# Performance work log

Measured on AMD Instinct MI355X. Metric: run time of the kernel, lower is better.

## Reference

```python
import jax, jax.numpy as jnp
import numpy as np

N_NODES = 100000
N_EDGES = 1600000
IN_DIM = 128
OUT_DIM = 64
SLOPE = 0.2


def setup_inputs() -> dict:
    key = jax.random.key(0)
    k1, k2, k3, k4 = jax.random.split(key, 4)
    h = jax.random.normal(k1, (N_NODES, IN_DIM), dtype=jnp.float32)
    W = jax.random.normal(k2, (OUT_DIM, IN_DIM), dtype=jnp.float32) * (1.0 / np.sqrt(IN_DIM))
    src = jax.random.randint(k3, (N_EDGES,), 0, N_NODES, dtype=jnp.int64)
    dst = jax.random.randint(k4, (N_EDGES,), 0, N_NODES, dtype=jnp.int64)
    return {"h": h, "W": W, "src": src, "dst": dst}


def reference(h, W, src, dst):
    n = h.shape[0]
    z = h @ W.T                                   # [N, out_dim]
    z_src = z[src]                                # [E, out_dim]
    z_dst = z[dst]                                # [E, out_dim]
    e = jax.nn.leaky_relu(jnp.sum(z_src * z_dst, axis=1), negative_slope=SLOPE)  # [E]
    # segment softmax over incoming edges of each destination node
    m = jax.ops.segment_max(e, dst, num_segments=n)        # [N], -inf for isolated nodes
    ex = jnp.exp(e - m[dst])                                # [E]
    denom = jax.ops.segment_sum(ex, dst, num_segments=n)    # [N]
    alpha = ex / denom[dst]                                 # [E]
    agg = jax.ops.segment_sum(alpha[:, None] * z_src, dst, num_segments=n)  # [N, out_dim]
    return jax.nn.elu(agg)
```

## Files before the change

kernel.cpp:

```cpp
#include <hip/hip_runtime.h>
#include <hip/hip_fp16.h>
#include <math.h>

#define SLOPE 0.2f
#define LOG2E 1.4426950408889634f

__device__ __forceinline__ unsigned short pk_f16(float x) {
    __half h = __float2half(x);
    return __half_as_ushort(h);
}
__device__ __forceinline__ float f16f(unsigned int bits_lo16) {
    return __half2float(__ushort_as_half((unsigned short)(bits_lo16 & 0xFFFFu)));
}

__global__ __launch_bounds__(256, 8) void gemm_hist_kernel(const float* __restrict__ h,
                                                           const float* __restrict__ W,
                                                           unsigned short* __restrict__ zh,
                                                           const int* __restrict__ dst,
                                                           int* __restrict__ cnt8,
                                                           unsigned short* __restrict__ rank,
                                                           int n, int ne) {
    int g = blockIdx.x / 3;
    int r = blockIdx.x % 3;
    if (r == 2) {
        int* __restrict__ cnt = cnt8 + (size_t)(g & 7) * n;
        int i = g * 256 + threadIdx.x;
        int base = i * 4;
        if (base + 3 < ne) {
            int4 d = *(const int4*)(dst + base);
            unsigned int r0 = atomicAdd(&cnt[d.x], 1);
            unsigned int r1 = atomicAdd(&cnt[d.y], 1);
            unsigned int r2 = atomicAdd(&cnt[d.z], 1);
            unsigned int r3 = atomicAdd(&cnt[d.w], 1);
            uint2 packed;
            packed.x = (r1 << 16) | (r0 & 0xFFFF);
            packed.y = (r3 << 16) | (r2 & 0xFFFF);
            *(uint2*)(rank + base) = packed;
        } else if (base < ne) {
            for (int rr = base; rr < ne; rr++)
                rank[rr] = (unsigned short)atomicAdd(&cnt[dst[rr]], 1);
        }
        return;
    }

    __shared__ float ws[128][36];
    int t = threadIdx.x;
    int gemmIdx = 2 * g + r;
    int nblk = gemmIdx >> 1;
    int ch0  = (gemmIdx & 1) << 5;
    const float4* __restrict__ W4 = reinterpret_cast<const float4*>(W);
#pragma unroll
    for (int j = 0; j < 4; j++) {
        int idx = t + j * 256;
        int o  = idx >> 5;
        int kq = idx & 31;
        float4 w = W4[(size_t)(ch0 + o) * 32 + kq];
        int k = kq << 2;
        int col = o ^ ((kq & 7) << 2);
        ws[k + 0][col] = w.x; ws[k + 1][col] = w.y;
        ws[k + 2][col] = w.z; ws[k + 3][col] = w.w;
    }
    __syncthreads();

    int ng = t >> 3, og = t & 7;
    int n0 = nblk * 64 + ng * 2;
    if (n0 >= n) return;
    const float* __restrict__ hp = h + (size_t)n0 * 128;

    float acc[2][4] = {};
#pragma unroll 4
    for (int k = 0; k < 128; k += 4) {
        int m = (k >> 2) & 7;
        int colb = (og ^ m) << 2;
        float4 hv[2], wv[4];
#pragma unroll
        for (int i = 0; i < 2; i++) hv[i] = *(const float4*)(hp + i * 128 + k);
#pragma unroll
        for (int kk = 0; kk < 4; kk++) wv[kk] = *(const float4*)&ws[k + kk][colb];
#pragma unroll
        for (int i = 0; i < 2; i++) {
            acc[i][0] += hv[i].x * wv[0].x + hv[i].y * wv[1].x + hv[i].z * wv[2].x + hv[i].w * wv[3].x;
            acc[i][1] += hv[i].x * wv[0].y + hv[i].y * wv[1].y + hv[i].z * wv[2].y + hv[i].w * wv[3].y;
            acc[i][2] += hv[i].x * wv[0].z + hv[i].y * wv[1].z + hv[i].z * wv[2].z + hv[i].w * wv[3].z;
            acc[i][3] += hv[i].x * wv[0].w + hv[i].y * wv[1].w + hv[i].z * wv[2].w + hv[i].w * wv[3].w;
        }
    }
#pragma unroll
    for (int i = 0; i < 2; i++) {
        ushort4 o4;
        o4.x = pk_f16(acc[i][0]);
        o4.y = pk_f16(acc[i][1]);
        o4.z = pk_f16(acc[i][2]);
        o4.w = pk_f16(acc[i][3]);
        *(ushort4*)&zh[(size_t)(n0 + i) * 64 + ch0 + og * 4] = o4;
    }
}

__global__ __launch_bounds__(256) void scan1(const int* __restrict__ cnt8,
                                             int* __restrict__ starts,
                                             int* __restrict__ bsums, int n) {
    __shared__ int ls[256];
    int tbase = blockIdx.x * 4096 + threadIdx.x * 16;
    int tot[16];
#pragma unroll
    for (int k = 0; k < 16; k++) tot[k] = 0;
    if (tbase + 15 < n) {
#pragma unroll
        for (int c = 0; c < 8; c++) {
            const int* cp = cnt8 + (size_t)c * n + tbase;
#pragma unroll
            for (int q = 0; q < 4; q++) {
                int4 v = *(const int4*)(cp + q * 4);
                tot[q * 4 + 0] += v.x; tot[q * 4 + 1] += v.y;
                tot[q * 4 + 2] += v.z; tot[q * 4 + 3] += v.w;
            }
        }
    } else {
        for (int k = 0; k < 16; k++) {
            int idx = tbase + k;
            if (idx < n)
                for (int c = 0; c < 8; c++) tot[k] += cnt8[(size_t)c * n + idx];
        }
    }
    int s = 0;
#pragma unroll
    for (int k = 0; k < 16; k++) s += tot[k];
    ls[threadIdx.x] = s;
    __syncthreads();
    for (int off = 1; off < 256; off <<= 1) {
        int t = threadIdx.x >= off ? ls[threadIdx.x - off] : 0;
        __syncthreads();
        ls[threadIdx.x] += t;
        __syncthreads();
    }
    int run = ls[threadIdx.x] - s;
    if (threadIdx.x == 255) bsums[blockIdx.x] = ls[255];
#pragma unroll
    for (int k = 0; k < 16; k++) {
        int idx = tbase + k;
        if (idx < n) starts[idx] = run;
        run += tot[k];
    }
}

__global__ __launch_bounds__(256) void scan3(int* __restrict__ starts,
                                             const int* __restrict__ bsums,
                                             int* __restrict__ cnt8,
                                             int n, int ne) {
    __shared__ int base_s;
    int i = blockIdx.x * 256 + threadIdx.x;
    if (threadIdx.x == 0) {
        int reg = (int)(blockIdx.x >> 4);
        int s = 0;
        for (int b = 0; b < reg; b++) s += bsums[b];
        base_s = s;
        if (blockIdx.x == 0) starts[n] = ne;
    }
    __syncthreads();
    if (i >= n) return;
    int b = starts[i] + base_s;
    starts[i] = b;
#pragma unroll
    for (int c = 0; c < 8; c++) {
        size_t off = (size_t)c * n + i;
        int t = cnt8[off];
        cnt8[off] = b;
        b += t;
    }
}

__global__ __launch_bounds__(256) void scatter8_kernel(const int* __restrict__ src,
                                                       const int* __restrict__ dst,
                                                       const int* __restrict__ cnt8,
                                                       const unsigned short* __restrict__ rank,
                                                       int* __restrict__ csr_src,
                                                       int n, int ne) {
    int i = blockIdx.x * 256 + threadIdx.x;
    int base = i * 8;
    if (base + 7 < ne) {
        const int* __restrict__ cb = cnt8 + (size_t)((base >> 10) & 7) * n;
        int4 s0 = *(const int4*)(src + base),  s1 = *(const int4*)(src + base + 4);
        int4 d0 = *(const int4*)(dst + base),  d1 = *(const int4*)(dst + base + 4);
        uint4 rp = *(const uint4*)(rank + base);
        csr_src[cb[d0.x] + (rp.x & 0xFFFF)] = s0.x;
        csr_src[cb[d0.y] + (rp.x >> 16)]    = s0.y;
        csr_src[cb[d0.z] + (rp.y & 0xFFFF)] = s0.z;
        csr_src[cb[d0.w] + (rp.y >> 16)]    = s0.w;
        csr_src[cb[d1.x] + (rp.z & 0xFFFF)] = s1.x;
        csr_src[cb[d1.y] + (rp.z >> 16)]    = s1.y;
        csr_src[cb[d1.z] + (rp.w & 0xFFFF)] = s1.z;
        csr_src[cb[d1.w] + (rp.w >> 16)]    = s1.w;
    } else {
        for (int e = base; e < ne; e++) {
            const int* cb = cnt8 + (size_t)((e >> 10) & 7) * n;
            csr_src[cb[dst[e]] + rank[e]] = src[e];
        }
    }
}

__global__ __launch_bounds__(256) void fused_node(const uint4* __restrict__ zh4,
                                                  const int* __restrict__ starts,
                                                  const int* __restrict__ csr_src,
                                                  float4* __restrict__ out4, int n) {
    int node = blockIdx.x * 4 + (threadIdx.x >> 6);
    if (node >= n) return;
    int lane = threadIdx.x & 63;
    int g = lane >> 3;
    int q = lane & 7;
    int rs = starts[node], re = starts[node + 1];

    uint4 zw = zh4[(size_t)node * 8 + q];
    float zdf[8];
    zdf[0] = f16f(zw.x); zdf[1] = f16f(zw.x >> 16);
    zdf[2] = f16f(zw.y); zdf[3] = f16f(zw.y >> 16);
    zdf[4] = f16f(zw.z); zdf[5] = f16f(zw.z >> 16);
    zdf[6] = f16f(zw.w); zdf[7] = f16f(zw.w >> 16);

    float m2 = -1e30f, denom = 0.f;
    float acc[8] = {};

    for (int c = rs; c < re; c += 64) {
        int j = c + lane;
        int sv = j < re ? csr_src[j] : 0;
        int cn = min(64, re - c);
        bool val0 = g < cn;
        int  s0 = __shfl(sv, val0 ? g : 0);
        uint4 w0 = zh4[(size_t)s0 * 8 + q];
        bool val1 = 8 + g < cn;
        int  s1 = __shfl(sv, val1 ? 8 + g : 0);
        uint4 w1 = zh4[(size_t)s1 * 8 + q];
        for (int k = 0; k < cn; k += 8) {
            int idx2 = k + 16 + g;
            bool val2 = idx2 < cn;
            int  s2 = __shfl(sv, val2 ? idx2 : 0);
            uint4 w2 = zh4[(size_t)s2 * 8 + q];

            float vf[8];
            vf[0] = f16f(w0.x); vf[1] = f16f(w0.x >> 16);
            vf[2] = f16f(w0.y); vf[3] = f16f(w0.y >> 16);
            vf[4] = f16f(w0.z); vf[5] = f16f(w0.z >> 16);
            vf[6] = f16f(w0.w); vf[7] = f16f(w0.w >> 16);

            float p = vf[0] * zdf[0];
#pragma unroll
            for (int jj = 1; jj < 8; jj++) p = fmaf(vf[jj], zdf[jj], p);
#pragma unroll
            for (int msk = 1; msk < 8; msk <<= 1) p += __shfl_xor(p, msk);

            float e = p > 0.f ? p : SLOPE * p;
            float e2 = e * LOG2E;
            e2 = val0 ? e2 : -2e30f;
            if (__any(e2 > m2)) {
                float mnew = fmaxf(m2, e2);
                float sc = exp2f(m2 - mnew);
                float ex = exp2f(e2 - mnew);
                denom = fmaf(denom, sc, ex);
#pragma unroll
                for (int jj = 0; jj < 8; jj++)
                    acc[jj] = fmaf(acc[jj], sc, ex * vf[jj]);
                m2 = mnew;
            } else {
                float ex = exp2f(e2 - m2);
                denom += ex;
#pragma unroll
                for (int jj = 0; jj < 8; jj++)
                    acc[jj] = fmaf(ex, vf[jj], acc[jj]);
            }
            w0 = w1; val0 = val1;
            w1 = w2; val1 = val2;
        }
    }
#pragma unroll
    for (int msk = 8; msk < 64; msk <<= 1) {
        float mo  = __shfl_xor(m2, msk);
        float dno = __shfl_xor(denom, msk);
        float ao[8];
#pragma unroll
        for (int jj = 0; jj < 8; jj++) ao[jj] = __shfl_xor(acc[jj], msk);
        float mnew = fmaxf(m2, mo);
        float ss = exp2f(m2 - mnew), so = exp2f(mo - mnew);
        denom = fmaf(denom, ss, dno * so);
#pragma unroll
        for (int jj = 0; jj < 8; jj++)
            acc[jj] = fmaf(acc[jj], ss, ao[jj] * so);
        m2 = mnew;
    }
    if (g == 0) {
        float inv = denom > 0.f ? 1.f / denom : 0.f;
        float r[8];
#pragma unroll
        for (int jj = 0; jj < 8; jj++) {
            float x = acc[jj] * inv;
            r[jj] = x > 0.f ? x : __expf(x) - 1.f;
        }
        out4[(size_t)node * 16 + q * 2 + 0] = make_float4(r[0], r[1], r[2], r[3]);
        out4[(size_t)node * 16 + q * 2 + 1] = make_float4(r[4], r[5], r[6], r[7]);
    }
}

extern "C" void kernel_launch(void* const* d_in, const int* in_sizes, int n_in,
                              void* d_out, int out_size, void* d_ws, size_t ws_size,
                              hipStream_t stream) {
    const float* h   = (const float*)d_in[0];
    const float* W   = (const float*)d_in[1];
    const int*   src = (const int*)d_in[2];
    const int*   dst = (const int*)d_in[3];
    int n  = in_sizes[0] / 128;
    int ne = in_sizes[2];

    unsigned short* zh      = (unsigned short*)d_ws;
    unsigned short* rank    = zh + (size_t)n * 64;
    int*            cnt8    = (int*)(rank + ne);
    int*            csr_src = cnt8 + (size_t)8 * n;
    int*            starts  = csr_src + ne;
    int*            bsums   = starts + ((n + 5) & ~3);

    int nbHist = (ne / 4 + 255) / 256;
    int nbTotal = nbHist * 3;
    int nb_scan = (n + 4095) / 4096;

    hipMemsetAsync(cnt8, 0, (size_t)8 * n * sizeof(int), stream);
    gemm_hist_kernel<<<nbTotal, 256, 0, stream>>>(h, W, zh, dst, cnt8, rank, n, ne);
    scan1<<<nb_scan, 256, 0, stream>>>(cnt8, starts, bsums, n);
    scan3<<<(n + 255) / 256, 256, 0, stream>>>(starts, bsums, cnt8, n, ne);
    scatter8_kernel<<<(ne / 8 + 255) / 256, 256, 0, stream>>>(src, dst, cnt8,
                                                              rank, csr_src, n, ne);
    fused_node<<<(n + 3) / 4, 256, 0, stream>>>((const uint4*)zh, starts, csr_src,
                                                (float4*)d_out, n);
}
```

Before: 192.0 us.

## Compute node projection with fp16 MFMA instead of scalar FMA

```diff
diff --git a/kernel.cpp b/kernel.cpp
--- a/kernel.cpp
+++ b/kernel.cpp
@@ -5,26 +5,41 @@
 #define SLOPE 0.2f
 #define LOG2E 1.4426950408889634f
 
+typedef _Float16 half8_t __attribute__((ext_vector_type(8)));
+typedef float    f32x4_t __attribute__((ext_vector_type(4)));
+
 __device__ __forceinline__ unsigned short pk_f16(float x) {
-    __half h = __float2half(x);
-    return __half_as_ushort(h);
+    return __half_as_ushort(__float2half(x));
 }
 __device__ __forceinline__ float f16f(unsigned int bits_lo16) {
     return __half2float(__ushort_as_half((unsigned short)(bits_lo16 & 0xFFFFu)));
 }
 
+__global__ __launch_bounds__(256) void wcvt_kernel(const float* __restrict__ W,
+                                                   unsigned short* __restrict__ Wh,
+                                                   int total4) {
+    int i = blockIdx.x * 256 + threadIdx.x;
+    if (i < total4) {
+        float4 w = *(const float4*)(W + (size_t)i * 4);
+        ushort4 o;
+        o.x = pk_f16(w.x); o.y = pk_f16(w.y);
+        o.z = pk_f16(w.z); o.w = pk_f16(w.w);
+        *(ushort4*)(Wh + (size_t)i * 4) = o;
+    }
+}
+
 __global__ __launch_bounds__(256, 8) void gemm_hist_kernel(const float* __restrict__ h,
-                                                           const float* __restrict__ W,
+                                                           const unsigned short* __restrict__ Wh,
                                                            unsigned short* __restrict__ zh,
                                                            const int* __restrict__ dst,
                                                            int* __restrict__ cnt8,
                                                            unsigned short* __restrict__ rank,
-                                                           int n, int ne) {
-    int g = blockIdx.x / 3;
-    int r = blockIdx.x % 3;
-    if (r == 2) {
-        int* __restrict__ cnt = cnt8 + (size_t)(g & 7) * n;
-        int i = g * 256 + threadIdx.x;
+                                                           int n, int ne, int nGemm) {
+    int r5 = blockIdx.x % 5;
+    int g5 = blockIdx.x / 5;
+    if (r5 == 4) {
+        int* __restrict__ cnt = cnt8 + (size_t)(g5 & 7) * n;
+        int i = g5 * 256 + threadIdx.x;
         int base = i * 4;
         if (base + 3 < ne) {
             int4 d = *(const int4*)(dst + base);
@@ -43,57 +58,35 @@
         return;
     }
 
-    __shared__ float ws[128][36];
-    int t = threadIdx.x;
-    int gemmIdx = 2 * g + r;
-    int nblk = gemmIdx >> 1;
-    int ch0  = (gemmIdx & 1) << 5;
-    const float4* __restrict__ W4 = reinterpret_cast<const float4*>(W);
-#pragma unroll
-    for (int j = 0; j < 4; j++) {
-        int idx = t + j * 256;
-        int o  = idx >> 5;
-        int kq = idx & 31;
-        float4 w = W4[(size_t)(ch0 + o) * 32 + kq];
-        int k = kq << 2;
-        int col = o ^ ((kq & 7) << 2);
-        ws[k + 0][col] = w.x; ws[k + 1][col] = w.y;
-        ws[k + 2][col] = w.z; ws[k + 3][col] = w.w;
-    }
-    __syncthreads();
-
-    int ng = t >> 3, og = t & 7;
-    int n0 = nblk * 64 + ng * 2;
+    int gemmIdx = g5 * 4 + r5;
+    int n0 = gemmIdx * 16;
     if (n0 >= n) return;
-    const float* __restrict__ hp = h + (size_t)n0 * 128;
-
-    float acc[2][4] = {};
-#pragma unroll 4
-    for (int k = 0; k < 128; k += 4) {
-        int m = (k >> 2) & 7;
-        int colb = (og ^ m) << 2;
-        float4 hv[2], wv[4];
-#pragma unroll
-        for (int i = 0; i < 2; i++) hv[i] = *(const float4*)(hp + i * 128 + k);
-#pragma unroll
-        for (int kk = 0; kk < 4; kk++) wv[kk] = *(const float4*)&ws[k + kk][colb];
-#pragma unroll
-        for (int i = 0; i < 2; i++) {
-            acc[i][0] += hv[i].x * wv[0].x + hv[i].y * wv[1].x + hv[i].z * wv[2].x + hv[i].w * wv[3].x;
-            acc[i][1] += hv[i].x * wv[0].y + hv[i].y * wv[1].y + hv[i].z * wv[2].y + hv[i].w * wv[3].y;
-            acc[i][2] += hv[i].x * wv[0].z + hv[i].y * wv[1].z + hv[i].z * wv[2].z + hv[i].w * wv[3].z;
-            acc[i][3] += hv[i].x * wv[0].w + hv[i].y * wv[1].w + hv[i].z * wv[2].w + hv[i].w * wv[3].w;
-        }
-    }
-#pragma unroll
-    for (int i = 0; i < 2; i++) {
-        ushort4 o4;
-        o4.x = pk_f16(acc[i][0]);
-        o4.y = pk_f16(acc[i][1]);
-        o4.z = pk_f16(acc[i][2]);
-        o4.w = pk_f16(acc[i][3]);
-        *(ushort4*)&zh[(size_t)(n0 + i) * 64 + ch0 + og * 4] = o4;
-    }
+    int lane = threadIdx.x & 63;
+    int wave = threadIdx.x >> 6;
+    int row = lane & 15;
+    int grp = lane >> 4;
+    int ch0 = wave * 16;
+
+    const float* __restrict__ hp = h + (size_t)(n0 + row) * 128 + grp * 8;
+    const unsigned short* __restrict__ wp = Wh + (size_t)(ch0 + row) * 128 + grp * 8;
+
+    f32x4_t acc = {0.f, 0.f, 0.f, 0.f};
+#pragma unroll
+    for (int c = 0; c < 4; c++) {
+        int kc = c * 32;
+        float4 a0 = *(const float4*)(hp + kc);
+        float4 a1 = *(const float4*)(hp + kc + 4);
+        half8_t av;
+        av[0] = (_Float16)a0.x; av[1] = (_Float16)a0.y;
+        av[2] = (_Float16)a0.z; av[3] = (_Float16)a0.w;
+        av[4] = (_Float16)a1.x; av[5] = (_Float16)a1.y;
+        av[6] = (_Float16)a1.z; av[7] = (_Float16)a1.w;
+        half8_t bv = *(const half8_t*)(wp + kc);
+        acc = __builtin_amdgcn_mfma_f32_16x16x32_f16(av, bv, acc, 0, 0, 0);
+    }
+#pragma unroll
+    for (int r = 0; r < 4; r++)
+        zh[(size_t)(n0 + grp * 4 + r) * 64 + ch0 + row] = pk_f16(acc[r]);
 }
 
 __global__ __launch_bounds__(256) void scan1(const int* __restrict__ cnt8,
@@ -312,15 +305,19 @@
     unsigned short* rank    = zh + (size_t)n * 64;
     int*            cnt8    = (int*)(rank + ne);
     int*            csr_src = cnt8 + (size_t)8 * n;
-    int*            starts  = csr_src + ne;
+    unsigned short* Wh      = (unsigned short*)(csr_src + ne);
+    int*            starts  = (int*)(Wh + 64 * 128);
     int*            bsums   = starts + ((n + 5) & ~3);
 
+    int nGemm = (n + 15) / 16;
     int nbHist = (ne / 4 + 255) / 256;
-    int nbTotal = nbHist * 3;
+    int nbTotal = nbHist * 5;
     int nb_scan = (n + 4095) / 4096;
 
     hipMemsetAsync(cnt8, 0, (size_t)8 * n * sizeof(int), stream);
-    gemm_hist_kernel<<<nbTotal, 256, 0, stream>>>(h, W, zh, dst, cnt8, rank, n, ne);
+    wcvt_kernel<<<(64 * 128 / 4 + 255) / 256, 256, 0, stream>>>(W, Wh, 64 * 128 / 4);
+    gemm_hist_kernel<<<nbTotal, 256, 0, stream>>>(h, Wh, zh, dst, cnt8, rank,
+                                                  n, ne, nGemm);
     scan1<<<nb_scan, 256, 0, stream>>>(cnt8, starts, bsums, n);
     scan3<<<(n + 255) / 256, 256, 0, stream>>>(starts, bsums, cnt8, n, ne);
     scatter8_kernel<<<(ne / 8 + 255) / 256, 256, 0, stream>>>(src, dst, cnt8,
```

Result: no change. 189.0 us (-1.5%).
